# Kernel optimization log

Measured on AMD Instinct MI355X. Metric: run time of the kernel, lower is better.

Reference implementation:

```python
import jax, jax.numpy as jnp
import numpy as np

# dims (see shape_source)
B, S, V, E, H, L, F = 512, 17, 40002, 1024, 16, 12, 4096
DH = E // H          # per-head dim = hidden_size // num_attention_heads
NREL = 500           # num_relations
NEDGE = 100          # num_edges (edge-label vocab)
BIG = 1000000.0


def _ln(x, g, b, eps):
    m = jnp.mean(x, axis=-1, keepdims=True)
    v = jnp.mean((x - m) ** 2, axis=-1, keepdims=True)
    return (x - m) * jax.lax.rsqrt(v + eps) * g + b


def setup_inputs() -> dict:
    key = jax.random.key(0)
    ks = jax.random.split(key, 24)
    n = lambda k, sh: 0.02 * jax.random.normal(k, sh, jnp.float32)
    inp = {
        # runtime inputs
        'input_ids': jax.random.randint(ks[0], (B, S), 0, V),
        'input_mask': jnp.ones((B, S), jnp.float32),
        'edge_labels': jax.random.randint(ks[1], (S, S), 0, NEDGE),
        'mask_pos': jax.random.randint(ks[2], (B,), 0, S),
        'mask_label': jax.random.randint(ks[3], (B,), 0, V),
        'mask_type': jnp.ones((B, 1), jnp.float32),  # +1 => entity slot masked
        'confidence': jax.random.uniform(ks[4], (B,), jnp.float32),
        # parameters
        'node_emb': n(ks[5], (V, E)),
        'edge_k': n(ks[6], (NEDGE, DH)),
        'edge_v': n(ks[7], (NEDGE, DH)),
        'ln1_g': jnp.ones((E,), jnp.float32), 'ln1_b': jnp.zeros((E,), jnp.float32),
        'Wq': n(ks[8], (L, E, E)), 'bq': jnp.zeros((L, E), jnp.float32),
        'Wk': n(ks[9], (L, E, E)), 'bk': jnp.zeros((L, E), jnp.float32),
        'Wv': n(ks[10], (L, E, E)), 'bv': jnp.zeros((L, E), jnp.float32),
        'Wo': n(ks[11], (L, E, E)), 'bo': jnp.zeros((L, E), jnp.float32),
        'lnA_g': jnp.ones((L, E), jnp.float32), 'lnA_b': jnp.zeros((L, E), jnp.float32),
        'W1': n(ks[12], (L, E, F)), 'b1': jnp.zeros((L, F), jnp.float32),
        'W2': n(ks[13], (L, F, E)), 'b2': jnp.zeros((L, E), jnp.float32),
        'lnF_g': jnp.ones((L, E), jnp.float32), 'lnF_b': jnp.zeros((L, E), jnp.float32),
        'ln2_g': jnp.ones((E,), jnp.float32), 'ln2_b': jnp.zeros((E,), jnp.float32),
        'fc2_bias': jnp.zeros((V,), jnp.float32),
    }
    return inp


def _forward(node_emb, edge_k, edge_v, ln1_g, ln1_b,
             Wq, bq, Wk, bk, Wv, bv, Wo, bo, lnA_g, lnA_b,
             W1, b1, W2, b2, lnF_g, lnF_b, ln2_g, ln2_b, fc2_bias,
             input_mask, mask_type, confidence,
             input_ids, edge_labels, mask_pos, mask_label):
    # embedding + pre-LN (dropout is identity in eval mode)
    x = _ln(node_emb[input_ids], ln1_g, ln1_b, 1e-12)          # [B,S,E]
    em = jnp.sign(edge_labels).astype(x.dtype)[:, :, None]     # [S,S,1]
    ek = edge_k[edge_labels] * em                              # [S,S,DH]
    ev = edge_v[edge_labels] * em
    m = input_mask[:, :, None]                                 # [B,S,1]
    attn_bias = (BIG * (m @ jnp.swapaxes(m, 1, 2) - 1.0))[:, None]  # [B,1,S,S]

    def step(h, p):
        wq, bq_, wk, bk_, wv, bv_, wo, bo_, ga, ba, w1, b1_, w2, b2_, gf, bf = p
        proj = lambda w, b: (h @ w + b).reshape(B, S, H, DH).transpose(0, 2, 1, 3)
        q = proj(wq, bq_) * (DH ** -0.5)
        k = proj(wk, bk_)
        v = proj(wv, bv_)
        # edge-aware attention scores: content + edge-key bias
        s = jnp.einsum('bhqd,bhkd->bhqk', q, k) \
            + jnp.einsum('bhqd,qkd->bhqk', q, ek) + attn_bias
        a = jax.nn.softmax(s, axis=-1)
        c = jnp.einsum('bhqk,bhkd->bhqd', a, v) \
            + jnp.einsum('bhqk,qkd->bhqd', a, ev)
        y = c.transpose(0, 2, 1, 3).reshape(B, S, E) @ wo + bo_
        h = _ln(h + y, ga, ba, 1e-12)                          # post-LN (cmd 'dan')
        f = jax.nn.gelu(h @ w1 + b1_, approximate=False) @ w2 + b2_
        return _ln(h + f, gf, bf, 1e-12), None

    enc, _ = jax.lax.scan(step, x, (Wq, bq, Wk, bk, Wv, bv, Wo, bo,
                                    lnA_g, lnA_b, W1, b1, W2, b2, lnF_g, lnF_b))

    # mode == 'normal': gather masked position (fc1 output is dead code in the original)
    hm = enc[jnp.arange(B), mask_pos]                          # [B,E]
    hm = _ln(jax.nn.gelu(hm, approximate=False), ln2_g, ln2_b, 1e-7)
    logits = hm @ node_emb.T + fc2_bias                        # tied projection [B,V]

    ti = jnp.concatenate([-jnp.ones((B, NREL), logits.dtype),
                          jnp.ones((B, V - NREL - 2), logits.dtype)], axis=1) * mask_type
    ti = jnp.concatenate([-jnp.ones((B, 2), logits.dtype), ti], axis=1)
    ti = jax.nn.relu(ti)                                       # candidate indicator [B,V]
    logits = logits + BIG * (ti - 1.0)

    oh = jax.nn.one_hot(mask_label, V, dtype=logits.dtype)
    ti2 = ti - oh
    num_cand = jnp.sum(ti2, axis=1)                            # [B]
    sl = ((1.0 + mask_type) * 0.9 + (1.0 - mask_type) * 0.9) / 2.0  # [B,1]
    soft = sl * oh + (1.0 - sl) * ti2 / num_cand[:, None]
    loss = jnp.mean(-jnp.sum(soft * jax.nn.log_softmax(logits, axis=1), axis=1) * confidence)
    return loss, logits


def reference(input_ids, input_mask, edge_labels, mask_pos, mask_label, mask_type,
              confidence, node_emb, edge_k, edge_v, ln1_g, ln1_b, Wq, bq, Wk, bk,
              Wv, bv, Wo, bo, lnA_g, lnA_b, W1, b1, W2, b2, lnF_g, lnF_b,
              ln2_g, ln2_b, fc2_bias):
    return _forward(node_emb, edge_k, edge_v, ln1_g, ln1_b, Wq, bq, Wk, bk, Wv, bv,
                    Wo, bo, lnA_g, lnA_b, W1, b1, W2, b2, lnF_g, lnF_b, ln2_g, ln2_b,
                    fc2_bias, input_mask, mask_type, confidence,
                    input_ids, edge_labels, mask_pos, mask_label)
```

## Files before the change

kernel.cpp:

```cpp
#include <hip/hip_runtime.h>
#include <hip/hip_bf16.h>

#define BB 512
#define SS 17
#define VV 40002
#define VPAD 40064
#define EE 1024
#define HH 16
#define LL 12
#define FF 4096
#define DHD 64
#define NRELC 500
#define MTOK (BB*SS)
#define BIGC 1000000.0f

typedef __bf16 bf16_t;
typedef __bf16 bf16x8 __attribute__((ext_vector_type(8)));
typedef __bf16 bf16x4 __attribute__((ext_vector_type(4)));
typedef float  f32x4  __attribute__((ext_vector_type(4)));

#define GLOAD_LDS16(g, l) __builtin_amdgcn_global_load_lds( \
    (const __attribute__((address_space(1))) void*)(g), \
    (__attribute__((address_space(3))) void*)(l), 16, 0, 0)

__device__ __forceinline__ float dgelu(float x) {
    return 0.5f * x * (1.f + erff(x * 0.70710678118654752f));
}

__device__ __forceinline__ float blk_sum(float v, float* sred) {
#pragma unroll
    for (int o = 32; o > 0; o >>= 1) v += __shfl_down(v, o);
    int lane = threadIdx.x & 63, w = threadIdx.x >> 6;
    __syncthreads();
    if (lane == 0) sred[w] = v;
    __syncthreads();
    return sred[0] + sred[1] + sred[2] + sred[3];
}
__device__ __forceinline__ float blk_max(float v, float* sred) {
#pragma unroll
    for (int o = 32; o > 0; o >>= 1) v = fmaxf(v, __shfl_down(v, o));
    int lane = threadIdx.x & 63, w = threadIdx.x >> 6;
    __syncthreads();
    if (lane == 0) sred[w] = v;
    __syncthreads();
    return fmaxf(fmaxf(sred[0], sred[1]), fmaxf(sred[2], sred[3]));
}

__global__ __launch_bounds__(256)
void edge_kernel(const int* __restrict__ labels, const float* __restrict__ eks,
                 const float* __restrict__ evs, float* __restrict__ ek,
                 float* __restrict__ ev) {
    int e = blockIdx.x * 256 + threadIdx.x;
    if (e >= SS * SS * DHD) return;
    int qk = e >> 6, d = e & 63;
    int lab = labels[qk];
    float sgn = lab > 0 ? 1.f : (lab < 0 ? -1.f : 0.f);
    ek[e] = eks[(size_t)lab * DHD + d] * sgn;
    ev[e] = evs[(size_t)lab * DHD + d] * sgn;
}

__global__ __launch_bounds__(256)
void embed_kernel(const int* __restrict__ ids, const float* __restrict__ emb,
                  const float* __restrict__ g, const float* __restrict__ bt,
                  bf16_t* __restrict__ out) {
    __shared__ float sred[4];
    int row = blockIdx.x;
    const float* src = emb + (size_t)ids[row] * EE;
    int c = threadIdx.x * 4;
    float4 x = *(const float4*)(src + c);
    float mean = blk_sum(x.x + x.y + x.z + x.w, sred) * (1.f / EE);
    float x0 = x.x - mean, x1 = x.y - mean, x2 = x.z - mean, x3 = x.w - mean;
    float var = blk_sum(x0*x0 + x1*x1 + x2*x2 + x3*x3, sred) * (1.f / EE);
    float rs = rsqrtf(var + 1e-12f);
    float4 gv = *(const float4*)(g + c), bv = *(const float4*)(bt + c);
    bf16x4 o;
    o[0] = (bf16_t)(x0*rs*gv.x + bv.x); o[1] = (bf16_t)(x1*rs*gv.y + bv.y);
    o[2] = (bf16_t)(x2*rs*gv.z + bv.z); o[3] = (bf16_t)(x3*rs*gv.w + bv.w);
    *(bf16x4*)(out + (size_t)row * EE + c) = o;
}

__global__ __launch_bounds__(256)
void resln_kernel(bf16_t* __restrict__ h, const bf16_t* __restrict__ y,
                  const float* __restrict__ g, const float* __restrict__ bt) {
    __shared__ float sred[4];
    int row = blockIdx.x; int c = threadIdx.x * 4;
    size_t off = (size_t)row * EE + c;
    bf16x4 a = *(const bf16x4*)(h + off), b4 = *(const bf16x4*)(y + off);
    float x0 = (float)a[0] + (float)b4[0], x1 = (float)a[1] + (float)b4[1];
    float x2 = (float)a[2] + (float)b4[2], x3 = (float)a[3] + (float)b4[3];
    float mean = blk_sum(x0 + x1 + x2 + x3, sred) * (1.f / EE);
    x0 -= mean; x1 -= mean; x2 -= mean; x3 -= mean;
    float var = blk_sum(x0*x0 + x1*x1 + x2*x2 + x3*x3, sred) * (1.f / EE);
    float rs = rsqrtf(var + 1e-12f);
    float4 gv = *(const float4*)(g + c), bv = *(const float4*)(bt + c);
    bf16x4 o;
    o[0] = (bf16_t)(x0*rs*gv.x + bv.x); o[1] = (bf16_t)(x1*rs*gv.y + bv.y);
    o[2] = (bf16_t)(x2*rs*gv.z + bv.z); o[3] = (bf16_t)(x3*rs*gv.w + bv.w);
    *(bf16x4*)(h + off) = o;
}

__global__ __launch_bounds__(256)
void hm_kernel(const bf16_t* __restrict__ h, const int* __restrict__ pos,
               const float* __restrict__ g, const float* __restrict__ bt,
               bf16_t* __restrict__ out) {
    __shared__ float sred[4];
    int b = blockIdx.x; int c = threadIdx.x * 4;
    const bf16_t* src = h + ((size_t)(b * SS + pos[b])) * EE + c;
    bf16x4 x = *(const bf16x4*)src;
    float x0 = dgelu((float)x[0]), x1 = dgelu((float)x[1]);
    float x2 = dgelu((float)x[2]), x3 = dgelu((float)x[3]);
    float mean = blk_sum(x0 + x1 + x2 + x3, sred) * (1.f / EE);
    x0 -= mean; x1 -= mean; x2 -= mean; x3 -= mean;
    float var = blk_sum(x0*x0 + x1*x1 + x2*x2 + x3*x3, sred) * (1.f / EE);
    float rs = rsqrtf(var + 1e-7f);
    float4 gv = *(const float4*)(g + c), bv = *(const float4*)(bt + c);
    bf16x4 o;
    o[0] = (bf16_t)(x0*rs*gv.x + bv.x); o[1] = (bf16_t)(x1*rs*gv.y + bv.y);
    o[2] = (bf16_t)(x2*rs*gv.z + bv.z); o[3] = (bf16_t)(x3*rs*gv.w + bv.w);
    *(bf16x4*)(out + (size_t)b * EE + c) = o;
}

__global__ __launch_bounds__(256)
void nodeconv_kernel(const float* __restrict__ src, bf16_t* __restrict__ dst) {
    const size_t total = (size_t)VPAD * (EE / 8);
    for (size_t idx = (size_t)blockIdx.x * 256 + threadIdx.x; idx < total;
         idx += (size_t)gridDim.x * 256) {
        size_t row = idx >> 7;
        bf16x8 o;
#pragma unroll
        for (int u = 0; u < 8; ++u) o[u] = (bf16_t)0.f;
        if (row < VV) {
            const float* s = src + (idx << 3);
            float4 a = *(const float4*)s, b = *(const float4*)(s + 4);
            o[0] = (bf16_t)a.x; o[1] = (bf16_t)a.y; o[2] = (bf16_t)a.z; o[3] = (bf16_t)a.w;
            o[4] = (bf16_t)b.x; o[5] = (bf16_t)b.y; o[6] = (bf16_t)b.z; o[7] = (bf16_t)b.w;
        }
        *(bf16x8*)(dst + (idx << 3)) = o;
    }
}

__global__ __launch_bounds__(256)
void transpose_kernel(const float* __restrict__ Wq, const float* __restrict__ Wk,
                      const float* __restrict__ Wv, const float* __restrict__ Wo,
                      const float* __restrict__ W1, const float* __restrict__ W2,
                      bf16_t* __restrict__ wt) {
    int t = blockIdx.x;
    const float* src; bf16_t* dst; int K, N, tile;
    if (t < 4096) {
        int mi = t >> 10; tile = t & 1023;
        src = mi == 0 ? Wq : mi == 1 ? Wk : mi == 2 ? Wv : Wo;
        dst = wt + (size_t)mi * (1u << 20);
        K = 1024; N = 1024;
    } else if (t < 8192) {
        tile = t - 4096; src = W1; dst = wt + (size_t)4 * (1u << 20); K = 1024; N = 4096;
    } else {
        tile = t - 8192; src = W2; dst = wt + (size_t)8 * (1u << 20); K = 4096; N = 1024;
    }
    int ntiles = N >> 5;
    int kt = tile / ntiles, nt = tile % ntiles;
    __shared__ float lds[32][33];
    int tx = threadIdx.x & 31, ty = threadIdx.x >> 5;
#pragma unroll
    for (int i = 0; i < 4; ++i) {
        int r = ty + i * 8;
        lds[r][tx] = src[(size_t)(kt * 32 + r) * N + nt * 32 + tx];
    }
    __syncthreads();
#pragma unroll
    for (int i = 0; i < 4; ++i) {
        int r = ty + i * 8;
        dst[(size_t)(nt * 32 + r) * K + kt * 32 + tx] = (bf16_t)lds[tx][r];
    }
}

template<int EPI, bool NB>
__global__ __launch_bounds__(256)
void gemm_bf16(const bf16_t* __restrict__ A, const bf16_t* __restrict__ B,
               const float* __restrict__ b0, const float* __restrict__ b1,
               const float* __restrict__ b2, const float* __restrict__ mt,
               void* __restrict__ Cout, int M, int N, int K) {
    __shared__ __align__(16) bf16_t sA[128 * 32];
    __shared__ __align__(16) bf16_t sB[128 * 32];
    const int tid = threadIdx.x;
    const int lane = tid & 63, wid = tid >> 6;
    const int wm = wid >> 1, wn = wid & 1;
    const int row16 = lane & 15, kblk = lane >> 4;

    const int nwg = gridDim.x * gridDim.y;
    const int wg = blockIdx.y * gridDim.x + blockIdx.x;
    const int q8 = nwg >> 3, r8 = nwg & 7;
    const int xcd = wg & 7, loc = wg >> 3;
    const int swz = (xcd < r8 ? xcd * (q8 + 1) : r8 * (q8 + 1) + (xcd - r8) * q8) + loc;
    const int bm = swz / gridDim.x, bn = swz % gridDim.x;

    f32x4 acc[4][4];
#pragma unroll
    for (int i = 0; i < 4; ++i)
#pragma unroll
        for (int j = 0; j < 4; ++j) acc[i][j] = (f32x4){0.f, 0.f, 0.f, 0.f};

    const bf16_t* Atile = A + (size_t)bm * 128 * K;
    const bf16_t* Btile = B + (size_t)bn * 128 * K;

    const int row_s0 = tid >> 2, chs0 = tid & 3;
    const int ch0 = chs0 ^ ((row_s0 >> 1) & 3);
    const int row_s1 = (256 + tid) >> 2, chs1 = tid & 3;
    const int ch1 = chs1 ^ ((row_s1 >> 1) & 3);
    bf16_t* ldsA0 = sA + ((size_t)(wid << 6) << 3);
    bf16_t* ldsA1 = sA + ((size_t)(256 + (wid << 6)) << 3);
    bf16_t* ldsB0 = sB + ((size_t)(wid << 6) << 3);
    bf16_t* ldsB1 = sB + ((size_t)(256 + (wid << 6)) << 3);

    for (int k0 = 0; k0 < K; k0 += 32) {
        GLOAD_LDS16(Atile + (size_t)row_s0 * K + k0 + ch0 * 8, ldsA0);
        GLOAD_LDS16(Atile + (size_t)row_s1 * K + k0 + ch1 * 8, ldsA1);
        GLOAD_LDS16(Btile + (size_t)row_s0 * K + k0 + ch0 * 8, ldsB0);
        GLOAD_LDS16(Btile + (size_t)row_s1 * K + k0 + ch1 * 8, ldsB1);
        __syncthreads();
        bf16x8 af[4], bfr[4];
#pragma unroll
        for (int i = 0; i < 4; ++i) {
            int r = wm * 64 + i * 16 + row16;
            af[i] = *(const bf16x8*)(sA + (((r << 2) | (kblk ^ ((r >> 1) & 3))) << 3));
        }
#pragma unroll
        for (int j = 0; j < 4; ++j) {
            int r = wn * 64 + j * 16 + row16;
            bfr[j] = *(const bf16x8*)(sB + (((r << 2) | (kblk ^ ((r >> 1) & 3))) << 3));
        }
#pragma unroll
        for (int i = 0; i < 4; ++i)
#pragma unroll
            for (int j = 0; j < 4; ++j)
                acc[i][j] = __builtin_amdgcn_mfma_f32_16x16x32_bf16(af[i], bfr[j], acc[i][j], 0, 0, 0);
        __syncthreads();
    }

    const int crow0 = bm * 128 + wm * 64;
    const int ccol0 = bn * 128 + wn * 64;
#pragma unroll
    for (int i = 0; i < 4; ++i) {
#pragma unroll
        for (int j = 0; j < 4; ++j) {
            int col = ccol0 + j * 16 + row16;
            if (NB && col >= N) continue;
            float bias, scale = 1.f;
            if (EPI == 4) {
                int seg = col >> 10;
                const float* bp = seg == 0 ? b0 : (seg == 1 ? b1 : b2);
                bias = bp[col & 1023];
                if (seg == 0) scale = 0.125f;
            } else {
                bias = b0[col];
            }
#pragma unroll
            for (int r = 0; r < 4; ++r) {
                int rowg = crow0 + i * 16 + kblk * 4 + r;
                float val = acc[i][j][r] + bias;
                if (EPI == 4) val *= scale;
                if (EPI == 2) val = dgelu(val);
                if (EPI == 3) {
                    float mtb = mt[rowg];
                    float t = (col < 2) ? 0.f : fmaxf(0.f, ((col - 2) < NRELC) ? -mtb : mtb);
                    val += BIGC * (t - 1.f);
                    ((float*)Cout)[(size_t)rowg * N + col] = val;
                } else {
                    ((bf16_t*)Cout)[(size_t)rowg * N + col] = (bf16_t)val;
                }
            }
        }
    }
}

__global__ __launch_bounds__(256)
void attn_kernel(const bf16_t* __restrict__ qkv, const float* __restrict__ ekb,
                 const float* __restrict__ evb, const float* __restrict__ mask,
                 bf16_t* __restrict__ ctx) {
    int bh = blockIdx.x; int b = bh >> 4; int h = bh & 15;
    __shared__ float sq[SS][DHD], sk[SS][DHD], sv[SS][DHD];
    __shared__ float ss[SS][SS + 1];
    __shared__ float sm[SS];
    int tid = threadIdx.x;
    for (int idx = tid; idx < 3 * SS * 8; idx += 256) {
        int t3 = idx / (SS * 8), rc = idx % (SS * 8), s = rc >> 3, c8 = rc & 7;
        bf16x8 v = *(const bf16x8*)(qkv + ((size_t)(b * SS + s)) * 3072 + t3 * 1024 + h * 64 + c8 * 8);
        float* dst = (t3 == 0 ? &sq[0][0] : t3 == 1 ? &sk[0][0] : &sv[0][0]) + s * 64 + c8 * 8;
#pragma unroll
        for (int u = 0; u < 8; ++u) dst[u] = (float)v[u];
    }
    if (tid < SS) sm[tid] = mask[b * SS + tid];
    __syncthreads();
    for (int e = tid; e < SS * SS; e += 256) {
        int qi = e / SS, ki = e % SS;
        const float* ek_ = ekb + (size_t)e * DHD;
        float acc = 0.f;
#pragma unroll 16
        for (int d = 0; d < DHD; ++d) acc += sq[qi][d] * (sk[ki][d] + ek_[d]);
        acc += BIGC * (sm[qi] * sm[ki] - 1.f);
        ss[qi][ki] = acc;
    }
    __syncthreads();
    if (tid < SS) {
        float mx = -1e30f;
        for (int ki = 0; ki < SS; ++ki) mx = fmaxf(mx, ss[tid][ki]);
        float sum = 0.f;
        for (int ki = 0; ki < SS; ++ki) { float e_ = expf(ss[tid][ki] - mx); sum += e_; ss[tid][ki] = e_; }
        float inv = 1.f / sum;
        for (int ki = 0; ki < SS; ++ki) ss[tid][ki] *= inv;
    }
    __syncthreads();
    for (int e = tid; e < SS * DHD; e += 256) {
        int qi = e >> 6, d = e & 63;
        float acc = 0.f;
#pragma unroll
        for (int ki = 0; ki < SS; ++ki)
            acc += ss[qi][ki] * (sv[ki][d] + evb[((size_t)(qi * SS + ki)) * DHD + d]);
        ctx[((size_t)(b * SS + qi)) * EE + h * DHD + d] = (bf16_t)acc;
    }
}

__global__ __launch_bounds__(256)
void loss_part_kernel(const float* __restrict__ logits, const float* __restrict__ mt,
                      const int* __restrict__ label, const float* __restrict__ conf,
                      float* __restrict__ lp) {
    __shared__ float sred[4];
    int b = blockIdx.x;
    const float* row = logits + (size_t)b * VV;
    float mx = -1e30f;
    for (int j = threadIdx.x; j < VV; j += 256) mx = fmaxf(mx, row[j]);
    mx = blk_max(mx, sred);
    float m = mt[b];
    float se = 0.f, s1 = 0.f, cnt = 0.f;
    for (int j = threadIdx.x; j < VV; j += 256) {
        float x = row[j];
        se += expf(x - mx);
        float t = (j < 2) ? 0.f : fmaxf(0.f, ((j - 2) < NRELC) ? -m : m);
        s1 += t * x;
        cnt += t;
    }
    se = blk_sum(se, sred);
    s1 = blk_sum(s1, sred);
    cnt = blk_sum(cnt, sred);
    if (threadIdx.x == 0) {
        float lse = mx + logf(se);
        float lsml = row[label[b]] - lse;
        float num_cand = cnt - 1.f;
        float v = 0.9f * lsml + 0.1f * ((s1 - cnt * lse) - lsml) / num_cand;
        lp[b] = -v * conf[b];
    }
}

__global__ __launch_bounds__(256)
void loss_reduce_kernel(const float* __restrict__ lp, float* __restrict__ out) {
    __shared__ float sred[4];
    float s = 0.f;
    for (int i = threadIdx.x; i < BB; i += 256) s += lp[i];
    s = blk_sum(s, sred);
    if (threadIdx.x == 0) out[0] = s * (1.f / BB);
}

extern "C" void kernel_launch(void* const* d_in, const int* in_sizes, int n_in,
                              void* d_out, int out_size, void* d_ws, size_t ws_size,
                              hipStream_t stream) {
    const int*   input_ids  = (const int*)d_in[0];
    const float* input_mask = (const float*)d_in[1];
    const int*   edge_lab   = (const int*)d_in[2];
    const int*   mask_pos   = (const int*)d_in[3];
    const int*   mask_label = (const int*)d_in[4];
    const float* mask_type  = (const float*)d_in[5];
    const float* confidence = (const float*)d_in[6];
    const float* node_emb   = (const float*)d_in[7];
    const float* edge_k     = (const float*)d_in[8];
    const float* edge_v     = (const float*)d_in[9];
    const float* ln1_g      = (const float*)d_in[10];
    const float* ln1_b      = (const float*)d_in[11];
    const float* Wq         = (const float*)d_in[12];
    const float* bq         = (const float*)d_in[13];
    const float* Wk         = (const float*)d_in[14];
    const float* bk         = (const float*)d_in[15];
    const float* Wv         = (const float*)d_in[16];
    const float* bv         = (const float*)d_in[17];
    const float* Wo         = (const float*)d_in[18];
    const float* bo         = (const float*)d_in[19];
    const float* lnA_g      = (const float*)d_in[20];
    const float* lnA_b      = (const float*)d_in[21];
    const float* W1         = (const float*)d_in[22];
    const float* b1         = (const float*)d_in[23];
    const float* W2         = (const float*)d_in[24];
    const float* b2         = (const float*)d_in[25];
    const float* lnF_g      = (const float*)d_in[26];
    const float* lnF_b      = (const float*)d_in[27];
    const float* ln2_g      = (const float*)d_in[28];
    const float* ln2_b      = (const float*)d_in[29];
    const float* fc2_bias   = (const float*)d_in[30];

    char* p = (char*)d_ws;
    bf16_t* wt    = (bf16_t*)p;
    size_t off = 25165824;
    bf16_t* hbuf  = (bf16_t*)(p + off); off += (size_t)MTOK * EE * 2;
    bf16_t* qkvb  = (bf16_t*)(p + off); off += (size_t)MTOK * FF * 2;
    bf16_t* cb    = (bf16_t*)(p + off); off += (size_t)MTOK * EE * 2;
    bf16_t* yb    = (bf16_t*)(p + off); off += (size_t)MTOK * EE * 2;
    float*  ekb   = (float*)(p + off);  off += (size_t)SS * SS * DHD * 4;
    float*  evb   = (float*)(p + off);  off += (size_t)SS * SS * DHD * 4;
    bf16_t* hmb   = (bf16_t*)(p + off); off += (size_t)BB * EE * 2;
    float*  lp    = (float*)(p + off);  off += (size_t)BB * 4;
    bf16_t* midb  = qkvb;
    bf16_t* nodeb = qkvb;

    float* loss_out   = (float*)d_out;
    float* logits_out = ((float*)d_out) + 1;

    edge_kernel<<<(SS * SS * DHD + 255) / 256, 256, 0, stream>>>(edge_lab, edge_k, edge_v, ekb, evb);
    embed_kernel<<<MTOK, 256, 0, stream>>>(input_ids, node_emb, ln1_g, ln1_b, hbuf);

    dim3 gqkv(3 * EE / 128, MTOK / 128);
    dim3 gproj(EE / 128, MTOK / 128);
    dim3 gffn1(FF / 128, MTOK / 128);

    for (int l = 0; l < LL; ++l) {
        size_t we = (size_t)l * EE * EE;
        size_t wf = (size_t)l * EE * FF;
        transpose_kernel<<<12288, 256, 0, stream>>>(Wq + we, Wk + we, Wv + we, Wo + we,
                                                    W1 + wf, W2 + wf, wt);
        gemm_bf16<4, false><<<gqkv, 256, 0, stream>>>(hbuf, wt,
            bq + (size_t)l * EE, bk + (size_t)l * EE, bv + (size_t)l * EE, nullptr,
            qkvb, MTOK, 3 * EE, EE);
        attn_kernel<<<BB * HH, 256, 0, stream>>>(qkvb, ekb, evb, input_mask, cb);
        gemm_bf16<0, false><<<gproj, 256, 0, stream>>>(cb, wt + (size_t)3 * (1u << 20),
            bo + (size_t)l * EE, nullptr, nullptr, nullptr, yb, MTOK, EE, EE);
        resln_kernel<<<MTOK, 256, 0, stream>>>(hbuf, yb, lnA_g + (size_t)l * EE, lnA_b + (size_t)l * EE);
        gemm_bf16<2, false><<<gffn1, 256, 0, stream>>>(hbuf, wt + (size_t)4 * (1u << 20),
            b1 + (size_t)l * FF, nullptr, nullptr, nullptr, midb, MTOK, FF, EE);
        gemm_bf16<0, false><<<gproj, 256, 0, stream>>>(midb, wt + (size_t)8 * (1u << 20),
            b2 + (size_t)l * EE, nullptr, nullptr, nullptr, yb, MTOK, EE, FF);
        resln_kernel<<<MTOK, 256, 0, stream>>>(hbuf, yb, lnF_g + (size_t)l * EE, lnF_b + (size_t)l * EE);
    }

    nodeconv_kernel<<<2048, 256, 0, stream>>>(node_emb, nodeb);
    hm_kernel<<<BB, 256, 0, stream>>>(hbuf, mask_pos, ln2_g, ln2_b, hmb);

    dim3 glog(VPAD / 128, BB / 128);
    gemm_bf16<3, true><<<glog, 256, 0, stream>>>(hmb, nodeb, fc2_bias, nullptr, nullptr,
        mask_type, logits_out, BB, VV, EE);

    loss_part_kernel<<<BB, 256, 0, stream>>>(logits_out, mask_type, mask_label, confidence, lp);
    loss_reduce_kernel<<<1, 256, 0, stream>>>(lp, loss_out);
}
```

Baseline: 5.993 ms.

## Add double-buffered 256x256 GEMM for QKV and FFN1 with tanh GELU

Adds a new 512-thread GEMM kernel with 256x256 output tiles, double-buffered LDS loads that prefetch the next K slice while the current one computes, and raised wave priority around the MFMA block. It is used for the QKV projection and the first FFN layer, which cuts redundant global loads per output and hides load latency. The FFN1 epilogue also switches from the erf GELU to a tanh-approximation GELU built on a fast exp, which is cheaper but changes numerics slightly. The larger tiles use more registers and LDS per block and produce fewer blocks, which can lower occupancy and leave the grid less evenly spread over the CUs.

```diff
diff --git a/kernel.cpp b/kernel.cpp
--- a/kernel.cpp
+++ b/kernel.cpp
@@ -25,6 +25,12 @@
 
 __device__ __forceinline__ float dgelu(float x) {
     return 0.5f * x * (1.f + erff(x * 0.70710678118654752f));
+}
+__device__ __forceinline__ float fgelu(float x) {
+    float y = 0.7978845608f * (x + 0.044715f * x * x * x);
+    float u = __expf(2.f * y);
+    float t = 1.f - 2.f / (u + 1.f);
+    return 0.5f * x * (1.f + t);
 }
 
 __device__ __forceinline__ float blk_sum(float v, float* sred) {
@@ -173,18 +179,18 @@
     }
 }
 
-template<int EPI, bool NB>
-__global__ __launch_bounds__(256)
-void gemm_bf16(const bf16_t* __restrict__ A, const bf16_t* __restrict__ B,
-               const float* __restrict__ b0, const float* __restrict__ b1,
-               const float* __restrict__ b2, const float* __restrict__ mt,
-               void* __restrict__ Cout, int M, int N, int K) {
-    __shared__ __align__(16) bf16_t sA[128 * 32];
-    __shared__ __align__(16) bf16_t sB[128 * 32];
+template<int EPI>
+__global__ __launch_bounds__(512)
+void gemm256(const bf16_t* __restrict__ A, const bf16_t* __restrict__ B,
+             const float* __restrict__ b0, const float* __restrict__ b1,
+             const float* __restrict__ b2, bf16_t* __restrict__ C,
+             int N, int K) {
+    __shared__ __align__(16) bf16_t sA[2 * 8192];
+    __shared__ __align__(16) bf16_t sB[2 * 8192];
     const int tid = threadIdx.x;
     const int lane = tid & 63, wid = tid >> 6;
-    const int wm = wid >> 1, wn = wid & 1;
-    const int row16 = lane & 15, kblk = lane >> 4;
+    const int wm = wid >> 2, wn = wid & 3;
+    const int r16 = lane & 15, kb = lane >> 4;
 
     const int nwg = gridDim.x * gridDim.y;
     const int wg = blockIdx.y * gridDim.x + blockIdx.x;
@@ -193,57 +199,76 @@
     const int swz = (xcd < r8 ? xcd * (q8 + 1) : r8 * (q8 + 1) + (xcd - r8) * q8) + loc;
     const int bm = swz / gridDim.x, bn = swz % gridDim.x;
 
-    f32x4 acc[4][4];
-#pragma unroll
-    for (int i = 0; i < 4; ++i)
+    f32x4 acc[8][4];
+#pragma unroll
+    for (int i = 0; i < 8; ++i)
 #pragma unroll
         for (int j = 0; j < 4; ++j) acc[i][j] = (f32x4){0.f, 0.f, 0.f, 0.f};
 
-    const bf16_t* Atile = A + (size_t)bm * 128 * K;
-    const bf16_t* Btile = B + (size_t)bn * 128 * K;
-
-    const int row_s0 = tid >> 2, chs0 = tid & 3;
-    const int ch0 = chs0 ^ ((row_s0 >> 1) & 3);
-    const int row_s1 = (256 + tid) >> 2, chs1 = tid & 3;
-    const int ch1 = chs1 ^ ((row_s1 >> 1) & 3);
-    bf16_t* ldsA0 = sA + ((size_t)(wid << 6) << 3);
-    bf16_t* ldsA1 = sA + ((size_t)(256 + (wid << 6)) << 3);
-    bf16_t* ldsB0 = sB + ((size_t)(wid << 6) << 3);
-    bf16_t* ldsB1 = sB + ((size_t)(256 + (wid << 6)) << 3);
-
-    for (int k0 = 0; k0 < K; k0 += 32) {
-        GLOAD_LDS16(Atile + (size_t)row_s0 * K + k0 + ch0 * 8, ldsA0);
-        GLOAD_LDS16(Atile + (size_t)row_s1 * K + k0 + ch1 * 8, ldsA1);
-        GLOAD_LDS16(Btile + (size_t)row_s0 * K + k0 + ch0 * 8, ldsB0);
-        GLOAD_LDS16(Btile + (size_t)row_s1 * K + k0 + ch1 * 8, ldsB1);
-        __syncthreads();
-        bf16x8 af[4], bfr[4];
-#pragma unroll
-        for (int i = 0; i < 4; ++i) {
-            int r = wm * 64 + i * 16 + row16;
-            af[i] = *(const bf16x8*)(sA + (((r << 2) | (kblk ^ ((r >> 1) & 3))) << 3));
+    const bf16_t* Atile = A + (size_t)bm * 256 * K;
+    const bf16_t* Btile = B + (size_t)bn * 256 * K;
+
+    const int g_ = (lane & 3) ^ ((lane >> 3) & 3);
+    const size_t soff0 = (size_t)(wid * 16 + (lane >> 2)) * K + g_ * 8;
+    const size_t soff1 = soff0 + (size_t)128 * K;
+    const int ldst0 = wid * 512;
+    const int ldst1 = 4096 + wid * 512;
+
+    int offA[8], offB[4];
+#pragma unroll
+    for (int i = 0; i < 8; ++i) {
+        int row = wm * 128 + i * 16 + r16;
+        offA[i] = row * 32 + ((kb ^ ((row >> 1) & 3)) << 3);
+    }
+#pragma unroll
+    for (int j = 0; j < 4; ++j) {
+        int row = wn * 64 + j * 16 + r16;
+        offB[j] = row * 32 + ((kb ^ ((row >> 1) & 3)) << 3);
+    }
+
+    GLOAD_LDS16(Atile + soff0, sA + ldst0);
+    GLOAD_LDS16(Atile + soff1, sA + ldst1);
+    GLOAD_LDS16(Btile + soff0, sB + ldst0);
+    GLOAD_LDS16(Btile + soff1, sB + ldst1);
+
+    const int nt = K >> 5;
+    for (int t = 0; t < nt; ++t) {
+        const int cur = (t & 1) << 13;
+        if (t + 1 < nt) {
+            const int nxt = ((t + 1) & 1) << 13;
+            const bf16_t* a_ = Atile + (size_t)(t + 1) * 32;
+            const bf16_t* b_ = Btile + (size_t)(t + 1) * 32;
+            GLOAD_LDS16(a_ + soff0, sA + nxt + ldst0);
+            GLOAD_LDS16(a_ + soff1, sA + nxt + ldst1);
+            GLOAD_LDS16(b_ + soff0, sB + nxt + ldst0);
+            GLOAD_LDS16(b_ + soff1, sB + nxt + ldst1);
+            asm volatile("s_waitcnt vmcnt(4)" ::: "memory");
+        } else {
+            asm volatile("s_waitcnt vmcnt(0)" ::: "memory");
         }
-#pragma unroll
-        for (int j = 0; j < 4; ++j) {
-            int r = wn * 64 + j * 16 + row16;
-            bfr[j] = *(const bf16x8*)(sB + (((r << 2) | (kblk ^ ((r >> 1) & 3))) << 3));
-        }
-#pragma unroll
-        for (int i = 0; i < 4; ++i)
+        asm volatile("s_barrier" ::: "memory");
+        bf16x8 af[8], bfr[4];
+#pragma unroll
+        for (int i = 0; i < 8; ++i) af[i] = *(const bf16x8*)(sA + cur + offA[i]);
+#pragma unroll
+        for (int j = 0; j < 4; ++j) bfr[j] = *(const bf16x8*)(sB + cur + offB[j]);
+        __builtin_amdgcn_s_setprio(1);
+#pragma unroll
+        for (int i = 0; i < 8; ++i)
 #pragma unroll
             for (int j = 0; j < 4; ++j)
                 acc[i][j] = __builtin_amdgcn_mfma_f32_16x16x32_bf16(af[i], bfr[j], acc[i][j], 0, 0, 0);
-        __syncthreads();
-    }
-
-    const int crow0 = bm * 128 + wm * 64;
-    const int ccol0 = bn * 128 + wn * 64;
-#pragma unroll
-    for (int i = 0; i < 4; ++i) {
+        __builtin_amdgcn_s_setprio(0);
+        asm volatile("s_barrier" ::: "memory");
+    }
+
+    const int crow0 = bm * 256 + wm * 128;
+    const int ccol0 = bn * 256 + wn * 64;
+#pragma unroll
+    for (int i = 0; i < 8; ++i) {
 #pragma unroll
         for (int j = 0; j < 4; ++j) {
-            int col = ccol0 + j * 16 + row16;
-            if (NB && col >= N) continue;
+            int col = ccol0 + j * 16 + r16;
             float bias, scale = 1.f;
             if (EPI == 4) {
                 int seg = col >> 10;
@@ -255,10 +280,91 @@
             }
 #pragma unroll
             for (int r = 0; r < 4; ++r) {
+                int rowg = crow0 + i * 16 + kb * 4 + r;
+                float val = acc[i][j][r] + bias;
+                if (EPI == 4) val *= scale;
+                if (EPI == 2) val = fgelu(val);
+                C[(size_t)rowg * N + col] = (bf16_t)val;
+            }
+        }
+    }
+}
+
+template<int EPI, bool NB>
+__global__ __launch_bounds__(256)
+void gemm_bf16(const bf16_t* __restrict__ A, const bf16_t* __restrict__ B,
+               const float* __restrict__ b0, const float* __restrict__ mt,
+               void* __restrict__ Cout, int M, int N, int K) {
+    __shared__ __align__(16) bf16_t sA[128 * 32];
+    __shared__ __align__(16) bf16_t sB[128 * 32];
+    const int tid = threadIdx.x;
+    const int lane = tid & 63, wid = tid >> 6;
+    const int wm = wid >> 1, wn = wid & 1;
+    const int row16 = lane & 15, kblk = lane >> 4;
+
+    const int nwg = gridDim.x * gridDim.y;
+    const int wg = blockIdx.y * gridDim.x + blockIdx.x;
+    const int q8 = nwg >> 3, r8 = nwg & 7;
+    const int xcd = wg & 7, loc = wg >> 3;
+    const int swz = (xcd < r8 ? xcd * (q8 + 1) : r8 * (q8 + 1) + (xcd - r8) * q8) + loc;
+    const int bm = swz / gridDim.x, bn = swz % gridDim.x;
+
+    f32x4 acc[4][4];
+#pragma unroll
+    for (int i = 0; i < 4; ++i)
+#pragma unroll
+        for (int j = 0; j < 4; ++j) acc[i][j] = (f32x4){0.f, 0.f, 0.f, 0.f};
+
+    const bf16_t* Atile = A + (size_t)bm * 128 * K;
+    const bf16_t* Btile = B + (size_t)bn * 128 * K;
+
+    const int row_s0 = tid >> 2, chs0 = tid & 3;
+    const int ch0 = chs0 ^ ((row_s0 >> 1) & 3);
+    const int row_s1 = (256 + tid) >> 2, chs1 = tid & 3;
+    const int ch1 = chs1 ^ ((row_s1 >> 1) & 3);
+    bf16_t* ldsA0 = sA + ((size_t)(wid << 6) << 3);
+    bf16_t* ldsA1 = sA + ((size_t)(256 + (wid << 6)) << 3);
+    bf16_t* ldsB0 = sB + ((size_t)(wid << 6) << 3);
+    bf16_t* ldsB1 = sB + ((size_t)(256 + (wid << 6)) << 3);
+
+    for (int k0 = 0; k0 < K; k0 += 32) {
+        GLOAD_LDS16(Atile + (size_t)row_s0 * K + k0 + ch0 * 8, ldsA0);
+        GLOAD_LDS16(Atile + (size_t)row_s1 * K + k0 + ch1 * 8, ldsA1);
+        GLOAD_LDS16(Btile + (size_t)row_s0 * K + k0 + ch0 * 8, ldsB0);
+        GLOAD_LDS16(Btile + (size_t)row_s1 * K + k0 + ch1 * 8, ldsB1);
+        __syncthreads();
+        bf16x8 af[4], bfr[4];
+#pragma unroll
+        for (int i = 0; i < 4; ++i) {
+            int r = wm * 64 + i * 16 + row16;
+            af[i] = *(const bf16x8*)(sA + (((r << 2) | (kblk ^ ((r >> 1) & 3))) << 3));
+        }
+#pragma unroll
+        for (int j = 0; j < 4; ++j) {
+            int r = wn * 64 + j * 16 + row16;
+            bfr[j] = *(const bf16x8*)(sB + (((r << 2) | (kblk ^ ((r >> 1) & 3))) << 3));
+        }
+#pragma unroll
+        for (int i = 0; i < 4; ++i)
+#pragma unroll
+            for (int j = 0; j < 4; ++j)
+                acc[i][j] = __builtin_amdgcn_mfma_f32_16x16x32_bf16(af[i], bfr[j], acc[i][j], 0, 0, 0);
+        __syncthreads();
+    }
+
+    const int crow0 = bm * 128 + wm * 64;
+    const int ccol0 = bn * 128 + wn * 64;
+#pragma unroll
+    for (int i = 0; i < 4; ++i) {
+#pragma unroll
+        for (int j = 0; j < 4; ++j) {
+            int col = ccol0 + j * 16 + row16;
+            if (NB && col >= N) continue;
+            float bias = b0[col];
+#pragma unroll
+            for (int r = 0; r < 4; ++r) {
                 int rowg = crow0 + i * 16 + kblk * 4 + r;
                 float val = acc[i][j][r] + bias;
-                if (EPI == 4) val *= scale;
-                if (EPI == 2) val = dgelu(val);
                 if (EPI == 3) {
                     float mtb = mt[rowg];
                     float t = (col < 2) ? 0.f : fmaxf(0.f, ((col - 2) < NRELC) ? -mtb : mtb);
@@ -414,26 +520,26 @@
     edge_kernel<<<(SS * SS * DHD + 255) / 256, 256, 0, stream>>>(edge_lab, edge_k, edge_v, ekb, evb);
     embed_kernel<<<MTOK, 256, 0, stream>>>(input_ids, node_emb, ln1_g, ln1_b, hbuf);
 
-    dim3 gqkv(3 * EE / 128, MTOK / 128);
+    dim3 gqkv(3 * EE / 256, MTOK / 256);
+    dim3 gffn1(FF / 256, MTOK / 256);
     dim3 gproj(EE / 128, MTOK / 128);
-    dim3 gffn1(FF / 128, MTOK / 128);
 
     for (int l = 0; l < LL; ++l) {
         size_t we = (size_t)l * EE * EE;
         size_t wf = (size_t)l * EE * FF;
         transpose_kernel<<<12288, 256, 0, stream>>>(Wq + we, Wk + we, Wv + we, Wo + we,
                                                     W1 + wf, W2 + wf, wt);
-        gemm_bf16<4, false><<<gqkv, 256, 0, stream>>>(hbuf, wt,
-            bq + (size_t)l * EE, bk + (size_t)l * EE, bv + (size_t)l * EE, nullptr,
-            qkvb, MTOK, 3 * EE, EE);
+        gemm256<4><<<gqkv, 512, 0, stream>>>(hbuf, wt,
+            bq + (size_t)l * EE, bk + (size_t)l * EE, bv + (size_t)l * EE,
+            qkvb, 3 * EE, EE);
         attn_kernel<<<BB * HH, 256, 0, stream>>>(qkvb, ekb, evb, input_mask, cb);
         gemm_bf16<0, false><<<gproj, 256, 0, stream>>>(cb, wt + (size_t)3 * (1u << 20),
-            bo + (size_t)l * EE, nullptr, nullptr, nullptr, yb, MTOK, EE, EE);
+            bo + (size_t)l * EE, nullptr, yb, MTOK, EE, EE);
         resln_kernel<<<MTOK, 256, 0, stream>>>(hbuf, yb, lnA_g + (size_t)l * EE, lnA_b + (size_t)l * EE);
-        gemm_bf16<2, false><<<gffn1, 256, 0, stream>>>(hbuf, wt + (size_t)4 * (1u << 20),
-            b1 + (size_t)l * FF, nullptr, nullptr, nullptr, midb, MTOK, FF, EE);
+        gemm256<2><<<gffn1, 512, 0, stream>>>(hbuf, wt + (size_t)4 * (1u << 20),
+            b1 + (size_t)l * FF, nullptr, nullptr, midb, FF, EE);
         gemm_bf16<0, false><<<gproj, 256, 0, stream>>>(midb, wt + (size_t)8 * (1u << 20),
-            b2 + (size_t)l * EE, nullptr, nullptr, nullptr, yb, MTOK, EE, FF);
+            b2 + (size_t)l * EE, nullptr, yb, MTOK, EE, FF);
         resln_kernel<<<MTOK, 256, 0, stream>>>(hbuf, yb, lnF_g + (size_t)l * EE, lnF_b + (size_t)l * EE);
     }
 
@@ -441,7 +547,7 @@
     hm_kernel<<<BB, 256, 0, stream>>>(hbuf, mask_pos, ln2_g, ln2_b, hmb);
 
     dim3 glog(VPAD / 128, BB / 128);
-    gemm_bf16<3, true><<<glog, 256, 0, stream>>>(hmb, nodeb, fc2_bias, nullptr, nullptr,
+    gemm_bf16<3, true><<<glog, 256, 0, stream>>>(hmb, nodeb, fc2_bias,
         mask_type, logits_out, BB, VV, EE);
 
     loss_part_kernel<<<BB, 256, 0, stream>>>(logits_out, mask_type, mask_label, confidence, lp);
```

Result: slower. 6.344 ms (+5.8%).

## Triple-buffer GEMM LDS tiles with async prefetch and use tanh GELU

Applied to the files above, without the earlier changes.

Rewrites the bf16 GEMM main loop to use three LDS stages. Global-to-LDS loads for tile t+2 are issued while MFMAs run on tile t, and `s_waitcnt vmcnt` plus one barrier per iteration replace the two `__syncthreads` calls. This is meant to hide global load latency behind matrix math, at the cost of three times the LDS per block, which may lower occupancy. It also precomputes the swizzled LDS fragment offsets outside the loop. Separately, it swaps the erf-based GELU in the FFN epilogue for a tanh approximation built on `__expf`, which changes the numerics slightly.

```diff
diff --git a/kernel.cpp b/kernel.cpp
--- a/kernel.cpp
+++ b/kernel.cpp
@@ -25,6 +25,12 @@
 
 __device__ __forceinline__ float dgelu(float x) {
     return 0.5f * x * (1.f + erff(x * 0.70710678118654752f));
+}
+__device__ __forceinline__ float fgelu(float x) {
+    float y = 0.7978845608f * (x + 0.044715f * x * x * x);
+    float u = __expf(2.f * y);
+    float t = 1.f - 2.f / (u + 1.f);
+    return 0.5f * x * (1.f + t);
 }
 
 __device__ __forceinline__ float blk_sum(float v, float* sred) {
@@ -179,8 +185,8 @@
                const float* __restrict__ b0, const float* __restrict__ b1,
                const float* __restrict__ b2, const float* __restrict__ mt,
                void* __restrict__ Cout, int M, int N, int K) {
-    __shared__ __align__(16) bf16_t sA[128 * 32];
-    __shared__ __align__(16) bf16_t sB[128 * 32];
+    __shared__ __align__(16) bf16_t sA[3 * 4096];
+    __shared__ __align__(16) bf16_t sB[3 * 4096];
     const int tid = threadIdx.x;
     const int lane = tid & 63, wid = tid >> 6;
     const int wm = wid >> 1, wn = wid & 1;
@@ -202,39 +208,71 @@
     const bf16_t* Atile = A + (size_t)bm * 128 * K;
     const bf16_t* Btile = B + (size_t)bn * 128 * K;
 
-    const int row_s0 = tid >> 2, chs0 = tid & 3;
-    const int ch0 = chs0 ^ ((row_s0 >> 1) & 3);
-    const int row_s1 = (256 + tid) >> 2, chs1 = tid & 3;
-    const int ch1 = chs1 ^ ((row_s1 >> 1) & 3);
-    bf16_t* ldsA0 = sA + ((size_t)(wid << 6) << 3);
-    bf16_t* ldsA1 = sA + ((size_t)(256 + (wid << 6)) << 3);
-    bf16_t* ldsB0 = sB + ((size_t)(wid << 6) << 3);
-    bf16_t* ldsB1 = sB + ((size_t)(256 + (wid << 6)) << 3);
-
-    for (int k0 = 0; k0 < K; k0 += 32) {
-        GLOAD_LDS16(Atile + (size_t)row_s0 * K + k0 + ch0 * 8, ldsA0);
-        GLOAD_LDS16(Atile + (size_t)row_s1 * K + k0 + ch1 * 8, ldsA1);
-        GLOAD_LDS16(Btile + (size_t)row_s0 * K + k0 + ch0 * 8, ldsB0);
-        GLOAD_LDS16(Btile + (size_t)row_s1 * K + k0 + ch1 * 8, ldsB1);
-        __syncthreads();
+    const int row_s0 = tid >> 2, chs = tid & 3;
+    const int ch0 = chs ^ ((row_s0 >> 1) & 3);
+    const int row_s1 = row_s0 + 64;
+    const int ch1 = chs ^ ((row_s1 >> 1) & 3);
+    const size_t soff0 = (size_t)row_s0 * K + ch0 * 8;
+    const size_t soff1 = (size_t)row_s1 * K + ch1 * 8;
+    const int ldo0 = wid * 512;
+    const int ldo1 = 2048 + wid * 512;
+
+    int offA[4], offB[4];
+#pragma unroll
+    for (int i = 0; i < 4; ++i) {
+        int r = wm * 64 + i * 16 + row16;
+        offA[i] = r * 32 + ((kblk ^ ((r >> 1) & 3)) << 3);
+    }
+#pragma unroll
+    for (int j = 0; j < 4; ++j) {
+        int r = wn * 64 + j * 16 + row16;
+        offB[j] = r * 32 + ((kblk ^ ((r >> 1) & 3)) << 3);
+    }
+
+#define STAGE_T(t_, buf_) do { \
+        const bf16_t* a_ = Atile + (size_t)(t_) * 32; \
+        const bf16_t* b_ = Btile + (size_t)(t_) * 32; \
+        bf16_t* dA = sA + (buf_) * 4096; \
+        bf16_t* dB = sB + (buf_) * 4096; \
+        GLOAD_LDS16(a_ + soff0, dA + ldo0); \
+        GLOAD_LDS16(a_ + soff1, dA + ldo1); \
+        GLOAD_LDS16(b_ + soff0, dB + ldo0); \
+        GLOAD_LDS16(b_ + soff1, dB + ldo1); \
+    } while (0)
+
+    const int nt = K >> 5;
+    STAGE_T(0, 0);
+    STAGE_T(1, 1);
+    asm volatile("s_waitcnt vmcnt(4)" ::: "memory");
+    __builtin_amdgcn_s_barrier();
+
+    int cur = 0, stg = 2;
+    for (int t = 0; t < nt; ++t) {
+        const bool more = (t + 2 < nt);
+        if (more) {
+            STAGE_T(t + 2, stg);
+            stg = (stg == 2) ? 0 : stg + 1;
+        }
+        const bf16_t* bufA = sA + cur * 4096;
+        const bf16_t* bufB = sB + cur * 4096;
         bf16x8 af[4], bfr[4];
 #pragma unroll
-        for (int i = 0; i < 4; ++i) {
-            int r = wm * 64 + i * 16 + row16;
-            af[i] = *(const bf16x8*)(sA + (((r << 2) | (kblk ^ ((r >> 1) & 3))) << 3));
-        }
-#pragma unroll
-        for (int j = 0; j < 4; ++j) {
-            int r = wn * 64 + j * 16 + row16;
-            bfr[j] = *(const bf16x8*)(sB + (((r << 2) | (kblk ^ ((r >> 1) & 3))) << 3));
-        }
+        for (int i = 0; i < 4; ++i) af[i] = *(const bf16x8*)(bufA + offA[i]);
+#pragma unroll
+        for (int j = 0; j < 4; ++j) bfr[j] = *(const bf16x8*)(bufB + offB[j]);
 #pragma unroll
         for (int i = 0; i < 4; ++i)
 #pragma unroll
             for (int j = 0; j < 4; ++j)
                 acc[i][j] = __builtin_amdgcn_mfma_f32_16x16x32_bf16(af[i], bfr[j], acc[i][j], 0, 0, 0);
-        __syncthreads();
-    }
+        if (t + 1 < nt) {
+            if (more) asm volatile("s_waitcnt vmcnt(4)" ::: "memory");
+            else      asm volatile("s_waitcnt vmcnt(0)" ::: "memory");
+            __builtin_amdgcn_s_barrier();
+        }
+        cur = (cur == 2) ? 0 : cur + 1;
+    }
+#undef STAGE_T
 
     const int crow0 = bm * 128 + wm * 64;
     const int ccol0 = bn * 128 + wn * 64;
@@ -258,11 +296,11 @@
                 int rowg = crow0 + i * 16 + kblk * 4 + r;
                 float val = acc[i][j][r] + bias;
                 if (EPI == 4) val *= scale;
-                if (EPI == 2) val = dgelu(val);
+                if (EPI == 2) val = fgelu(val);
                 if (EPI == 3) {
                     float mtb = mt[rowg];
-                    float t = (col < 2) ? 0.f : fmaxf(0.f, ((col - 2) < NRELC) ? -mtb : mtb);
-                    val += BIGC * (t - 1.f);
+                    float tt = (col < 2) ? 0.f : fmaxf(0.f, ((col - 2) < NRELC) ? -mtb : mtb);
+                    val += BIGC * (tt - 1.f);
                     ((float*)Cout)[(size_t)rowg * N + col] = val;
                 } else {
                     ((bf16_t*)Cout)[(size_t)rowg * N + col] = (bf16_t)val;
```

New measurement: 5.562 ms (median of 2 runs). -7.2%, faster.
